# Kernel tuning notes

Measured on AMD Instinct MI355X. Metric: run time of the kernel, lower is better.

Reference implementation:

```python
import jax, jax.numpy as jnp
import numpy as np

M0, M1, H = 128, 64, 8            # scalar mul, vector mul, num heads
AH0, AH1 = 16, 8                  # per-head irreps: 16x0e + 8x1e
D = M0 + 3 * M1                   # 320 node feature dim
DTP0 = M0 + M1                    # 192 scalar channels out of depthwise TP
DTP1 = M0 + 2 * M1                # 256 vector channels out of depthwise TP
WNUM = 2 * M0 + 3 * M1            # 448 TP path weights (uvu, edge mul=1)
RAD_IN, RAD_HID = 32, 64
N_NODES, N_EDGES = 10000, 160000
INV_SQRT3 = 1.0 / np.sqrt(3.0)    # CG norm for 1e x 1e -> 0e
INV_SQRT2 = 1.0 / np.sqrt(2.0)    # CG norm for 1e x 1e -> 1e


def _split(x, m0, m1):
    # e3nn layout: [m0 scalars | m1 vectors * 3 components]
    return x[..., :m0], x[..., m0:].reshape(x.shape[:-1] + (m1, 3))


def _silu(x):
    return x * jax.nn.sigmoid(x)


def _smooth_leaky(x, a=0.2):
    # SmoothLeakyReLU from equiformer
    return 0.5 * (1 + a) * x + 0.5 * (1 - a) * x * (2.0 * jax.nn.sigmoid(x) - 1.0)


def _dtp(s, v, e0, e1, w):
    # depthwise (uvu) tensor product of (M0x0e + M1x1e) with edge attr (1x0e + 1x1e)
    # s [E,M0], v [E,M1,3], e0 [E,1], e1 [E,3], w [E,WNUM] or [WNUM] (internal)
    w1, w2, w3, w4, w5 = jnp.split(w, [M0, 2 * M0, 2 * M0 + M1, 2 * M0 + 2 * M1], axis=-1)
    os1 = w1 * s * e0                                                  # 0e x 0e -> 0e
    os2 = w4 * (jnp.einsum('emc,ec->em', v, e1) * INV_SQRT3)           # 1e x 1e -> 0e
    ov1 = (w2 * s)[..., None] * e1[:, None, :]                         # 0e x 1e -> 1e
    ov2 = w3[..., None] * v * e0[..., None]                            # 1e x 0e -> 1e
    ov3 = w5[..., None] * (jnp.cross(v, e1[:, None, :]) * INV_SQRT2)   # 1e x 1e -> 1e
    return jnp.concatenate([os1, os2], -1), jnp.concatenate([ov1, ov2, ov3], -2)


def _forward(node_input, edge_src, edge_dst, edge_attr, edge_scalars,
             Wsrc_s, Wsrc_v, bsrc, Wdst_s, Wdst_v,
             rad_W1, rad_b1, rad_W2, rad_off,
             Wact_s, bact, Wact_v, Walpha, balpha, w_int,
             Wval_s, bval, Wval_v, alpha_dot, Wproj_s, bproj, Wproj_v):
    N = node_input.shape[0]
    E = edge_src.shape[0]
    s, v = _split(node_input, M0, M1)
    # merge_src / merge_dst: per-irrep linear (bias only on scalars of src)
    ms_s = s @ Wsrc_s + bsrc
    ms_v = jnp.einsum('nmc,mk->nkc', v, Wsrc_v)
    md_s = s @ Wdst_s
    md_v = jnp.einsum('nmc,mk->nkc', v, Wdst_v)
    msg_s = ms_s[edge_src] + md_s[edge_dst]          # [E, M0]
    msg_v = ms_v[edge_src] + md_v[edge_dst]          # [E, M1, 3]
    e0, e1 = edge_attr[:, :1], edge_attr[:, 1:4]
    # radial profile MLP -> edge-dependent TP weights
    w = _silu(edge_scalars @ rad_W1 + rad_b1) @ rad_W2 + rad_off       # [E, WNUM]
    ds, dv = _dtp(msg_s, msg_v, e0, e1, w)           # [E, DTP0], [E, DTP1, 3]
    # alpha branch: linear on TP scalars -> heads -> smooth leaky -> dot
    al = _smooth_leaky((ds @ Walpha + balpha).reshape(E, H, AH0))
    logits = jnp.einsum('ehk,hk->eh', al, alpha_dot[0])                # [E, H]
    # value branch: sep_act.lin + gate
    scal = ds @ Wact_s + bact                        # [E, M0+M1] scalars+gates
    gated_v = jnp.einsum('emc,mk->ekc', dv, Wact_v)  # [E, M1, 3]
    val_s = _silu(scal[:, :M0])
    val_v = gated_v * jax.nn.sigmoid(scal[:, M0:])[..., None]
    # sep_value: depthwise TP with internal weights + linear
    vs, vv = _dtp(val_s, val_v, e0, e1, w_int)
    out_s = vs @ Wval_s + bval                       # [E, H*AH0]
    out_v = jnp.einsum('emc,mk->ekc', vv, Wval_v)    # [E, H*AH1, 3]
    value = jnp.concatenate([out_s.reshape(E, H, AH0),
                             out_v.reshape(E, H, AH1 * 3)], axis=2)    # [E, H, 40]
    # softmax over incoming edges per destination node
    mx = jax.lax.stop_gradient(jax.ops.segment_max(logits, edge_dst, num_segments=N))
    mx = jnp.where(jnp.isfinite(mx), mx, 0.0)
    ex = jnp.exp(logits - mx[edge_dst])
    den = jax.ops.segment_sum(ex, edge_dst, num_segments=N)
    alpha = ex / (den[edge_dst] + 1e-16)             # [E, H]
    agg = jax.ops.segment_sum(value * alpha[..., None], edge_dst, num_segments=N)
    # heads2vec + output projection
    node_s = agg[:, :, :AH0].reshape(N, H * AH0)
    node_v = agg[:, :, AH0:].reshape(N, H * AH1, 3)
    po_s = node_s @ Wproj_s + bproj
    po_v = jnp.einsum('nmc,mk->nkc', node_v, Wproj_v)
    return jnp.concatenate([po_s, po_v.reshape(N, M1 * 3)], axis=1)


def _lin(key, fi, fo):
    return jax.random.normal(key, (fi, fo), jnp.float32) / np.sqrt(fi)


def setup_inputs() -> dict:
    ks = iter(jax.random.split(jax.random.key(0), 40))
    inp = {}
    inp['node_input'] = jax.random.normal(next(ks), (N_NODES, D), jnp.float32)
    inp['edge_src'] = jax.random.randint(next(ks), (N_EDGES,), 0, N_NODES)
    inp['edge_dst'] = jax.random.randint(next(ks), (N_EDGES,), 0, N_NODES)
    inp['edge_attr'] = jax.random.normal(next(ks), (N_EDGES, 4), jnp.float32)
    inp['edge_scalars'] = jax.random.normal(next(ks), (N_EDGES, RAD_IN), jnp.float32)
    inp['Wsrc_s'] = _lin(next(ks), M0, M0)
    inp['Wsrc_v'] = _lin(next(ks), M1, M1)
    inp['bsrc'] = 0.1 * jax.random.normal(next(ks), (M0,), jnp.float32)
    inp['Wdst_s'] = _lin(next(ks), M0, M0)
    inp['Wdst_v'] = _lin(next(ks), M1, M1)
    inp['rad_W1'] = _lin(next(ks), RAD_IN, RAD_HID)
    inp['rad_b1'] = 0.1 * jax.random.normal(next(ks), (RAD_HID,), jnp.float32)
    inp['rad_W2'] = _lin(next(ks), RAD_HID, WNUM)
    inp['rad_off'] = 0.1 * jax.random.normal(next(ks), (WNUM,), jnp.float32)
    inp['Wact_s'] = _lin(next(ks), DTP0, M0 + M1)
    inp['bact'] = 0.1 * jax.random.normal(next(ks), (M0 + M1,), jnp.float32)
    inp['Wact_v'] = _lin(next(ks), DTP1, M1)
    inp['Walpha'] = _lin(next(ks), DTP0, H * AH0)
    inp['balpha'] = 0.1 * jax.random.normal(next(ks), (H * AH0,), jnp.float32)
    inp['w_int'] = jax.random.normal(next(ks), (WNUM,), jnp.float32)
    inp['Wval_s'] = _lin(next(ks), DTP0, H * AH0)
    inp['bval'] = 0.1 * jax.random.normal(next(ks), (H * AH0,), jnp.float32)
    inp['Wval_v'] = _lin(next(ks), DTP1, H * AH1)
    inp['alpha_dot'] = jax.random.normal(next(ks), (1, H, AH0), jnp.float32) / np.sqrt(AH0)
    inp['Wproj_s'] = _lin(next(ks), H * AH0, M0)
    inp['bproj'] = 0.1 * jax.random.normal(next(ks), (M0,), jnp.float32)
    inp['Wproj_v'] = _lin(next(ks), H * AH1, M1)
    return inp


def reference(node_input, edge_src, edge_dst, edge_attr, edge_scalars,
              Wsrc_s, Wsrc_v, bsrc, Wdst_s, Wdst_v,
              rad_W1, rad_b1, rad_W2, rad_off,
              Wact_s, bact, Wact_v, Walpha, balpha, w_int,
              Wval_s, bval, Wval_v, alpha_dot, Wproj_s, bproj, Wproj_v):
    return _forward(node_input, edge_src, edge_dst, edge_attr, edge_scalars,
                    Wsrc_s, Wsrc_v, bsrc, Wdst_s, Wdst_v,
                    rad_W1, rad_b1, rad_W2, rad_off,
                    Wact_s, bact, Wact_v, Walpha, balpha, w_int,
                    Wval_s, bval, Wval_v, alpha_dot, Wproj_s, bproj, Wproj_v)
```

## Files before the change

kernel.cpp:

```cpp
#include <hip/hip_runtime.h>

#define NN 10000
#define NE 160000
#define INV_SQRT3f 0.57735026918962576f
#define INV_SQRT2f 0.70710678118654752f

typedef short bshort8 __attribute__((ext_vector_type(8)));
typedef float floatx4 __attribute__((ext_vector_type(4)));
#define MFMA16(a,b,c) __builtin_amdgcn_mfma_f32_16x16x32_bf16((a),(b),(c),0,0,0)

__device__ __forceinline__ float sigm(float x){ return 1.f/(1.f+__expf(-x)); }
__device__ __forceinline__ float siluf(float x){ return x*sigm(x); }
__device__ __forceinline__ float sleaky(float x){ return 0.6f*x + 0.4f*x*(2.f*sigm(x)-1.f); }
__device__ __forceinline__ unsigned short f2bf(float f){
  return (unsigned short)((__float_as_uint(f) + 0x8000u)>>16);
}
__device__ __forceinline__ float bf2f(unsigned short h){
  return __uint_as_float(((unsigned)h)<<16);
}
__device__ __forceinline__ unsigned cvtpk(float lo, float hi){
  unsigned r;
  asm("v_cvt_pk_bf16_f32 %0, %1, %2" : "=v"(r) : "v"(lo), "v"(hi));
  return r;
}
__device__ __forceinline__ float lo16f(unsigned u){ return __uint_as_float(u<<16); }
__device__ __forceinline__ float hi16f(unsigned u){ return __uint_as_float(u & 0xffff0000u); }

#define O_W1   0
#define O_W2   2048
#define O_WAS  30720
#define O_WAVT 67584
#define O_WAVB 75776
#define O_WVS  83968
#define O_WVVT 108544
#define O_WVVB 116736
#define O_WALP 124928
#define SWZ_TOTAL 149504

__global__ __launch_bounds__(256) void k_pre_all(
    const float* __restrict__ x,
    const float* __restrict__ Wsrc_s, const float* __restrict__ Wsrc_v,
    const float* __restrict__ bsrc,
    const float* __restrict__ Wdst_s, const float* __restrict__ Wdst_v,
    unsigned short* __restrict__ ms_s, unsigned short* __restrict__ md_s,
    unsigned short* __restrict__ ms_v, unsigned short* __restrict__ md_v,
    const float* __restrict__ W1, const float* __restrict__ W2,
    const float* __restrict__ WAs, const float* __restrict__ WAv,
    const float* __restrict__ WVs, const float* __restrict__ WVv,
    const float* __restrict__ WAl, const float* __restrict__ w_int,
    unsigned short* __restrict__ swz,
    float* __restrict__ num, float* __restrict__ den, int* __restrict__ cnt) {
  __shared__ __align__(16) float s_s[128*16];
  __shared__ __align__(16) float s_v[192*16];
  const int tid = threadIdx.x;
  const int b = blockIdx.x;
  if (b >= 1209) {
    int base = (b-1209)*256 + tid;
    float4 z = {0.f,0.f,0.f,0.f};
    for (int i = base; i < 800000; i += 554496) ((float4*)num)[i] = z;
    if (base < 20000) ((float4*)den)[base] = z;
    if (base < 10000) cnt[base] = 0;
    return;
  }
  if (b >= 625) {
    int s = (b-625)*256 + tid;
    if (s >= SWZ_TOTAL) return;
    const float* src; int base, N, KT, rowOff;
    if      (s < 2048)  { base=O_W1;   src=W1;  N=64;  KT=1; rowOff=0; }
    else if (s < 30720) { base=O_W2;   src=W2;  N=448; KT=2; rowOff=0; }
    else if (s < 67584) { base=O_WAS;  src=WAs; N=192; KT=6; rowOff=0; }
    else if (s < 75776) { base=O_WAVT; src=WAv; N=64;  KT=4; rowOff=0; }
    else if (s < 83968) { base=O_WAVB; src=WAv; N=64;  KT=4; rowOff=128; }
    else if (s < 108544){ base=O_WVS;  src=WVs; N=128; KT=6; rowOff=0; }
    else if (s < 116736){ base=O_WVVT; src=WVv; N=64;  KT=4; rowOff=0; }
    else if (s < 124928){ base=O_WVVB; src=WVv; N=64;  KT=4; rowOff=128; }
    else                { base=O_WALP; src=WAl; N=128; KT=6; rowOff=0; }
    int loc = s - base;
    int j = loc & 7, l = (loc>>3)&63, kt = (loc>>9)%KT, nt = loc/(512*KT);
    int row = kt*32 + (l>>4)*8 + j + rowOff;
    int col = nt*16 + (l&15);
    float scl = 1.f;
    if      (base == O_WVS)  scl = (row < 128) ? w_int[row] : w_int[192+row]*INV_SQRT3f;
    else if (base == O_WVVT) scl = w_int[128+row];
    else if (base == O_WVVB) scl = (row < 192) ? w_int[128+row] : w_int[192+row]*INV_SQRT2f;
    swz[s] = f2bf(src[row*N + col] * scl);
    return;
  }
  const int n0 = b*16;
  for (int idx = tid; idx < 16*320; idx += 256) {
    int n = idx/320, d = idx - n*320;
    float val = x[(n0+n)*320 + d];
    if (d < 128) s_s[d*16+n] = val;
    else         s_v[(d-128)*16+n] = val;
  }
  __syncthreads();
  {
    int g = tid>>7, j = tid&127;
    float accs[8], accd[8];
    float bb = bsrc[j];
    #pragma unroll
    for (int i=0;i<8;i++){ accs[i]=bb; accd[i]=0.f; }
    for (int k=0;k<128;k++) {
      float w1 = Wsrc_s[k*128+j], w2 = Wdst_s[k*128+j];
      float4 a0 = *(const float4*)&s_s[k*16+g*8];
      float4 a1 = *(const float4*)&s_s[k*16+g*8+4];
      accs[0]+=a0.x*w1; accs[1]+=a0.y*w1; accs[2]+=a0.z*w1; accs[3]+=a0.w*w1;
      accs[4]+=a1.x*w1; accs[5]+=a1.y*w1; accs[6]+=a1.z*w1; accs[7]+=a1.w*w1;
      accd[0]+=a0.x*w2; accd[1]+=a0.y*w2; accd[2]+=a0.z*w2; accd[3]+=a0.w*w2;
      accd[4]+=a1.x*w2; accd[5]+=a1.y*w2; accd[6]+=a1.z*w2; accd[7]+=a1.w*w2;
    }
    #pragma unroll
    for (int i=0;i<8;i++){ int n=n0+g*8+i; ms_s[n*128+j]=f2bf(accs[i]); md_s[n*128+j]=f2bf(accd[i]); }
  }
  if (tid < 192) {
    int c = tid>>6, k = tid&63;
    #pragma unroll
    for (int half=0; half<2; ++half) {
      float accs[8], accd[8];
      #pragma unroll
      for (int e=0;e<8;e++){ accs[e]=0.f; accd[e]=0.f; }
      for (int m=0;m<64;m++) {
        float w1 = Wsrc_v[m*64+k], w2 = Wdst_v[m*64+k];
        float4 v0 = *(const float4*)&s_v[(m*3+c)*16 + half*8];
        float4 v1 = *(const float4*)&s_v[(m*3+c)*16 + half*8 + 4];
        accs[0]+=v0.x*w1; accs[1]+=v0.y*w1; accs[2]+=v0.z*w1; accs[3]+=v0.w*w1;
        accs[4]+=v1.x*w1; accs[5]+=v1.y*w1; accs[6]+=v1.z*w1; accs[7]+=v1.w*w1;
        accd[0]+=v0.x*w2; accd[1]+=v0.y*w2; accd[2]+=v0.z*w2; accd[3]+=v0.w*w2;
        accd[4]+=v1.x*w2; accd[5]+=v1.y*w2; accd[6]+=v1.z*w2; accd[7]+=v1.w*w2;
      }
      #pragma unroll
      for (int e=0;e<8;e++){
        int n = n0 + half*8 + e;
        ms_v[(n*64+k)*4 + c] = f2bf(accs[e]);
        md_v[(n*64+k)*4 + c] = f2bf(accd[e]);
      }
    }
  }
}

__global__ __launch_bounds__(256) void k_hist(const int* __restrict__ edst,
                                              int* __restrict__ cnt) {
  int e = blockIdx.x*256 + threadIdx.x;
  if (e < NE) atomicAdd(&cnt[edst[e]], 1);
}

__global__ __launch_bounds__(256) void k_scan(const int* __restrict__ cnt,
                                              int* __restrict__ offs) {
  __shared__ int sc[10240];
  __shared__ int wsum[4];
  const int tid = threadIdx.x;
  const int lane = tid & 63, wave = tid >> 6;
  for (int i = tid; i < 10240; i += 256) sc[i] = (i < NN) ? cnt[i] : 0;
  __syncthreads();
  int v[40]; int s = 0;
  #pragma unroll
  for (int j=0;j<40;j++){ v[j] = sc[tid*40+j]; s += v[j]; }
  int incl = s;
  #pragma unroll
  for (int d=1; d<64; d<<=1) { int t = __shfl_up(incl, d, 64); if (lane>=d) incl += t; }
  if (lane==63) wsum[wave] = incl;
  __syncthreads();
  int wbase = 0;
  for (int w=0; w<wave; ++w) wbase += wsum[w];
  int excl = wbase + incl - s;
  #pragma unroll
  for (int j=0;j<40;j++){ int i = tid*40+j; if (i<NN) offs[i] = excl; excl += v[j]; }
}

__global__ __launch_bounds__(256) void k_scatter(const int* __restrict__ edst,
                                                 int* __restrict__ offs,
                                                 int* __restrict__ perm) {
  int e = blockIdx.x*256 + threadIdx.x;
  if (e < NE) {
    int pos = atomicAdd(&offs[edst[e]], 1);
    perm[pos] = e;
  }
}

__global__ __launch_bounds__(256, 6) void e_all(
    const unsigned short* __restrict__ ms_s, const unsigned short* __restrict__ md_s,
    const unsigned short* __restrict__ ms_v, const unsigned short* __restrict__ md_v,
    const int* __restrict__ esrc, const int* __restrict__ edst,
    const int* __restrict__ perm,
    const float* __restrict__ eattr, const float* __restrict__ escal,
    const float* __restrict__ rad_b1, const float* __restrict__ rad_off,
    const float* __restrict__ bact,
    const float* __restrict__ bval,
    const float* __restrict__ balpha, const float* __restrict__ alpha_dot,
    const unsigned short* __restrict__ swz,
    float* __restrict__ den, float* __restrict__ num) {
  __shared__ __align__(16) char smem[24768];
  unsigned short* ads  = (unsigned short*)smem;
  unsigned short* at1  = (unsigned short*)(smem+6400);
  unsigned short* advb = (unsigned short*)(smem+10752);
  unsigned short* aes  = (unsigned short*)(smem+10752);
  unsigned short* ah   = (unsigned short*)(smem+12032);
  float* vout          = (float*)(smem+10752);
  float* s_e0 = (float*)(smem+23808);
  float* s_e1 = (float*)(smem+23872);
  float* s_ex = (float*)(smem+24064);
  int* s_eid  = (int*)(smem+24576);
  int* s_src  = (int*)(smem+24640);
  int* s_dst  = (int*)(smem+24704);
  const int tid  = threadIdx.x;
  const int lane = tid & 63, wave = tid >> 6;
  const int quad = lane >> 4, l15 = lane & 15;
  const int bswz = (blockIdx.x & 7)*1250 + (blockIdx.x >> 3);
  const int eb = bswz*16;

  if (tid < 16) {
    int eid = perm[eb+tid];
    s_eid[tid] = eid; s_src[tid] = esrc[eid]; s_dst[tid] = edst[eid];
  }
  __syncthreads();
  if (tid >= 64 && tid < 128) {
    int t = tid-64, e = t>>2, q = t&3;
    float a = eattr[s_eid[e]*4+q];
    if (q == 0) s_e0[e] = a; else s_e1[(q-1)*16+e] = a;
  }
  {
    int e = tid>>4, i0 = (tid&15)*2;
    float2 es = *(const float2*)&escal[s_eid[e]*32+i0];
    *(unsigned*)&aes[e*40+i0] = cvtpk(es.x, es.y);
  }
  __syncthreads();

  {
    int nt = wave, col = nt*16 + l15;
    bshort8 a = *(const bshort8*)&aes[l15*40 + quad*8];
    bshort8 b = *(const bshort8*)&swz[O_W1 + (nt*64 + lane)*8];
    float bb = rad_b1[col];
    floatx4 acc = {bb,bb,bb,bb};
    acc = MFMA16(a, b, acc);
    #pragma unroll
    for (int r=0;r<4;r++) ah[(quad*4+r)*72 + col] = f2bf(siluf(acc[r]));
  }
  __syncthreads();

  {
    bshort8 ha0 = *(const bshort8*)&ah[l15*72 + quad*8];
    bshort8 ha1 = *(const bshort8*)&ah[l15*72 + 32 + quad*8];
    __syncthreads();
    int src_[4], dst_[4];
    #pragma unroll
    for (int r=0;r<4;r++){ int e=quad*4+r; src_[r]=s_src[e]; dst_[r]=s_dst[e]; }
    #pragma unroll
    for (int p=0;p<2;p++) {
      int nt1 = wave*2+p, nt2 = nt1+8;
      int m = nt1*16 + l15;
      float o1 = rad_off[m], o2 = rad_off[128+m];
      floatx4 a1 = {o1,o1,o1,o1}, a2 = {o2,o2,o2,o2};
      a1 = MFMA16(ha0, *(const bshort8*)&swz[O_W2 + ((nt1*2+0)*64+lane)*8], a1);
      a1 = MFMA16(ha1, *(const bshort8*)&swz[O_W2 + ((nt1*2+1)*64+lane)*8], a1);
      a2 = MFMA16(ha0, *(const bshort8*)&swz[O_W2 + ((nt2*2+0)*64+lane)*8], a2);
      a2 = MFMA16(ha1, *(const bshort8*)&swz[O_W2 + ((nt2*2+1)*64+lane)*8], a2);
      #pragma unroll
      for (int r=0;r<4;r++) {
        int e = quad*4+r;
        float msgs = bf2f(ms_s[src_[r]*128+m]) + bf2f(md_s[dst_[r]*128+m]);
        ads[e*200+m] = f2bf(a1[r]*msgs*s_e0[e]);
        at1[e*136+m] = f2bf(a2[r]*msgs);
      }
    }
    floatx4 aw3, aw4, aw5;
    {
      int nt = 16 + wave; float o = rad_off[nt*16+l15];
      floatx4 acc = {o,o,o,o};
      acc = MFMA16(ha0, *(const bshort8*)&swz[O_W2 + ((nt*2+0)*64+lane)*8], acc);
      acc = MFMA16(ha1, *(const bshort8*)&swz[O_W2 + ((nt*2+1)*64+lane)*8], acc);
      aw3 = acc;
    }
    {
      int nt = 20 + wave; float o = rad_off[nt*16+l15];
      floatx4 acc = {o,o,o,o};
      acc = MFMA16(ha0, *(const bshort8*)&swz[O_W2 + ((nt*2+0)*64+lane)*8], acc);
      acc = MFMA16(ha1, *(const bshort8*)&swz[O_W2 + ((nt*2+1)*64+lane)*8], acc);
      aw4 = acc;
    }
    {
      int nt = 24 + wave; float o = rad_off[nt*16+l15];
      floatx4 acc = {o,o,o,o};
      acc = MFMA16(ha0, *(const bshort8*)&swz[O_W2 + ((nt*2+0)*64+lane)*8], acc);
      acc = MFMA16(ha1, *(const bshort8*)&swz[O_W2 + ((nt*2+1)*64+lane)*8], acc);
      aw5 = acc;
    }
    const int k = wave*16 + l15;
    #pragma unroll
    for (int r=0;r<4;r++) {
      int e = quad*4 + r;
      uint2 us = *(const uint2*)&ms_v[(src_[r]*64 + k)*4];
      uint2 ud = *(const uint2*)&md_v[(dst_[r]*64 + k)*4];
      float vx = lo16f(us.x) + lo16f(ud.x);
      float vy = hi16f(us.x) + hi16f(ud.x);
      float vz = lo16f(us.y) + lo16f(ud.y);
      float ex1 = s_e1[0+e], ey1 = s_e1[16+e], ez1 = s_e1[32+e];
      float e0 = s_e0[e];
      float d = vx*ex1 + vy*ey1 + vz*ez1;
      ads[e*200+128+k] = f2bf(aw4[r]*d*INV_SQRT3f);
      float w3v = aw3[r]*e0;
      float w5  = aw5[r]*INV_SQRT2f;
      advb[0*2176 + e*136 + k] = f2bf(w3v*vx);
      advb[1*2176 + e*136 + k] = f2bf(w3v*vy);
      advb[2*2176 + e*136 + k] = f2bf(w3v*vz);
      advb[0*2176 + e*136 + 64+k] = f2bf(w5*(vy*ez1 - vz*ey1));
      advb[1*2176 + e*136 + 64+k] = f2bf(w5*(vz*ex1 - vx*ez1));
      advb[2*2176 + e*136 + 64+k] = f2bf(w5*(vx*ey1 - vy*ex1));
    }
  }
  __syncthreads();

  floatx4 sc0, sc1, sc2, gsa, gb0, gb1, gb2;
  {
    bshort8 fa[6];
    #pragma unroll
    for (int kt=0;kt<6;kt++) fa[kt] = *(const bshort8*)&ads[l15*200 + kt*32 + quad*8];
    #pragma unroll
    for (int t=0;t<2;t++) {
      int h = wave*2 + t;
      int col = h*16 + l15;
      float bb = balpha[col];
      floatx4 acc = {bb,bb,bb,bb};
      #pragma unroll
      for (int kt=0;kt<6;kt++)
        acc = MFMA16(fa[kt], *(const bshort8*)&swz[O_WALP + ((h*6+kt)*64+lane)*8], acc);
      float ad = alpha_dot[col];
      float exv[4];
      #pragma unroll
      for (int r=0;r<4;r++) {
        float p = sleaky(acc[r])*ad;
        p += __shfl_xor(p, 1);
        p += __shfl_xor(p, 2);
        p += __shfl_xor(p, 4);
        p += __shfl_xor(p, 8);
        float ex = __expf(p);
        exv[r] = ex;
        if (l15 == 0) s_ex[(quad*4+r)*8+h] = ex;
      }
      if (l15 == 0) {
        float racc = exv[0]; int cur = s_dst[quad*4];
        #pragma unroll
        for (int r=1;r<4;r++) {
          int d = s_dst[quad*4+r];
          if (d != cur) { atomicAdd(&den[cur*8+h], racc); racc = 0.f; cur = d; }
          racc += exv[r];
        }
        atomicAdd(&den[cur*8+h], racc);
      }
    }
    {
      float bb = bact[wave*16 + l15];
      floatx4 a0 = {bb,bb,bb,bb};
      #pragma unroll
      for (int kt=0;kt<6;kt++)
        a0 = MFMA16(fa[kt], *(const bshort8*)&swz[O_WAS + ((wave*6+kt)*64+lane)*8], a0);
      sc0 = a0;
    }
    {
      float bb = bact[(wave+4)*16 + l15];
      floatx4 a1 = {bb,bb,bb,bb};
      #pragma unroll
      for (int kt=0;kt<6;kt++)
        a1 = MFMA16(fa[kt], *(const bshort8*)&swz[O_WAS + (((wave+4)*6+kt)*64+lane)*8], a1);
      sc1 = a1;
    }
    {
      float bb = bact[(wave+8)*16 + l15];
      floatx4 a2 = {bb,bb,bb,bb};
      #pragma unroll
      for (int kt=0;kt<6;kt++)
        a2 = MFMA16(fa[kt], *(const bshort8*)&swz[O_WAS + (((wave+8)*6+kt)*64+lane)*8], a2);
      sc2 = a2;
    }
    bshort8 ft[4];
    #pragma unroll
    for (int kt=0;kt<4;kt++) ft[kt] = *(const bshort8*)&at1[l15*136 + kt*32 + quad*8];
    {
      floatx4 acc = {0.f,0.f,0.f,0.f};
      #pragma unroll
      for (int kt=0;kt<4;kt++)
        acc = MFMA16(ft[kt], *(const bshort8*)&swz[O_WAVT + ((wave*4+kt)*64+lane)*8], acc);
      gsa = acc;
    }
    {
      bshort8 wb[4];
      #pragma unroll
      for (int kt=0;kt<4;kt++) wb[kt] = *(const bshort8*)&swz[O_WAVB + ((wave*4+kt)*64+lane)*8];
      #pragma unroll
      for (int c=0;c<3;c++) {
        floatx4 acc = {0.f,0.f,0.f,0.f};
        #pragma unroll
        for (int kt=0;kt<4;kt++) {
          bshort8 fb = *(const bshort8*)&advb[c*2176 + l15*136 + kt*32 + quad*8];
          acc = MFMA16(fb, wb[kt], acc);
        }
        if (c==0) gb0 = acc; else if (c==1) gb1 = acc; else gb2 = acc;
      }
    }
  }
  __syncthreads();

  {
    const int k = wave*16 + l15;
    #pragma unroll
    for (int r=0;r<4;r++) {
      int row = quad*4 + r;
      float e0 = s_e0[row];
      {
        float v = siluf(sc0[r]);
        ads[row*200+k] = f2bf(v*e0);
        at1[row*136+k] = f2bf(v);
      }
      {
        float v = siluf(sc1[r]);
        ads[row*200+64+k] = f2bf(v*e0);
        at1[row*136+64+k] = f2bf(v);
      }
      {
        float sg = sigm(sc2[r]);
        float gs = gsa[r];
        float ex1 = s_e1[0+row], ey1 = s_e1[16+row], ez1 = s_e1[32+row];
        float v0 = (gs*ex1 + gb0[r])*sg;
        float v1 = (gs*ey1 + gb1[r])*sg;
        float v2 = (gs*ez1 + gb2[r])*sg;
        float d = v0*ex1 + v1*ey1 + v2*ez1;
        ads[row*200+128+k] = f2bf(d);
        advb[0*2176 + row*136 + k] = f2bf(v0*e0);
        advb[1*2176 + row*136 + k] = f2bf(v1*e0);
        advb[2*2176 + row*136 + k] = f2bf(v2*e0);
        advb[0*2176 + row*136 + 64+k] = f2bf(v1*ez1 - v2*ey1);
        advb[1*2176 + row*136 + 64+k] = f2bf(v2*ex1 - v0*ez1);
        advb[2*2176 + row*136 + 64+k] = f2bf(v0*ey1 - v1*ex1);
      }
    }
  }
  __syncthreads();

  {
    bshort8 ft[4];
    #pragma unroll
    for (int kt=0;kt<4;kt++) ft[kt] = *(const bshort8*)&at1[l15*136 + kt*32 + quad*8];
    floatx4 vsh = {0.f,0.f,0.f,0.f};
    #pragma unroll
    for (int kt=0;kt<4;kt++)
      vsh = MFMA16(ft[kt], *(const bshort8*)&swz[O_WVVT + ((wave*4+kt)*64+lane)*8], vsh);
    floatx4 vb0, vb1, vb2;
    {
      bshort8 wb[4];
      #pragma unroll
      for (int kt=0;kt<4;kt++) wb[kt] = *(const bshort8*)&swz[O_WVVB + ((wave*4+kt)*64+lane)*8];
      #pragma unroll
      for (int c=0;c<3;c++) {
        floatx4 acc = {0.f,0.f,0.f,0.f};
        #pragma unroll
        for (int kt=0;kt<4;kt++) {
          bshort8 fb = *(const bshort8*)&advb[c*2176 + l15*136 + kt*32 + quad*8];
          acc = MFMA16(fb, wb[kt], acc);
        }
        if (c==0) vb0 = acc; else if (c==1) vb1 = acc; else vb2 = acc;
      }
    }
    __syncthreads();
    const int k = wave*16 + l15;
    const int h = k>>3, q = k&7;
    #pragma unroll
    for (int r=0;r<4;r++) {
      int row = quad*4 + r;
      float exr = s_ex[row*8+h];
      vout[row*194 + h*24 + q*3 + 0] = (vb0[r] + s_e1[0*16+row]*vsh[r])*exr;
      vout[row*194 + h*24 + q*3 + 1] = (vb1[r] + s_e1[1*16+row]*vsh[r])*exr;
      vout[row*194 + h*24 + q*3 + 2] = (vb2[r] + s_e1[2*16+row]*vsh[r])*exr;
    }
  }
  __syncthreads();

  if (tid < 192) {
    const int jj = tid;
    const int h = jj/24, rr = jj - h*24;
    float acc = 0.f; int cur = s_dst[0];
    #pragma unroll
    for (int e = 0; e < 16; ++e) {
      int d = s_dst[e];
      if (d != cur) { atomicAdd(&num[cur*320 + h*40 + 16 + rr], acc); acc = 0.f; cur = d; }
      acc += vout[e*194 + jj];
    }
    atomicAdd(&num[cur*320 + h*40 + 16 + rr], acc);
  }
  __syncthreads();

  {
    bshort8 fa[6];
    #pragma unroll
    for (int kt=0;kt<6;kt++) fa[kt] = *(const bshort8*)&ads[l15*200 + kt*32 + quad*8];
    #pragma unroll
    for (int t=0;t<2;t++) {
      int h = wave + 4*t;
      float bb = bval[h*16 + l15];
      floatx4 acc = {bb,bb,bb,bb};
      #pragma unroll
      for (int kt=0;kt<6;kt++)
        acc = MFMA16(fa[kt], *(const bshort8*)&swz[O_WVS + ((h*6+kt)*64+lane)*8], acc);
      #pragma unroll
      for (int r=0;r<4;r++) {
        int row = quad*4 + r;
        vout[row*132 + h*16 + l15] = acc[r]*s_ex[row*8+h];
      }
    }
  }
  __syncthreads();

  if (tid < 128) {
    const int j = tid, h = j>>4, jj = j&15;
    float acc = 0.f; int cur = s_dst[0];
    #pragma unroll
    for (int e = 0; e < 16; ++e) {
      int d = s_dst[e];
      if (d != cur) { atomicAdd(&num[cur*320 + h*40 + jj], acc); acc = 0.f; cur = d; }
      acc += vout[e*132 + j];
    }
    atomicAdd(&num[cur*320 + h*40 + jj], acc);
  }
}

__global__ __launch_bounds__(256) void node_post(
    const float* __restrict__ num, const float* __restrict__ den,
    const float* __restrict__ Wproj_s, const float* __restrict__ bproj,
    const float* __restrict__ Wproj_v, float* __restrict__ out) {
  __shared__ __align__(16) float s_ns[128*16];
  __shared__ __align__(16) float s_nv[192*16];
  const int tid = threadIdx.x;
  const int n0 = blockIdx.x*16;
  for (int idx = tid; idx < 16*320; idx += 256) {
    int n = idx/320, j = idx - n*320;
    int h = j/40, r = j - h*40;
    float a = num[(n0+n)*320+j] / (den[(n0+n)*8+h] + 1e-16f);
    if (r < 16) s_ns[(h*16+r)*16+n] = a;
    else        s_nv[(h*24 + (r-16))*16+n] = a;
  }
  __syncthreads();
  {
    int g = tid>>7, j = tid&127;
    float acc[8]; float b = bproj[j];
    #pragma unroll
    for (int i=0;i<8;i++) acc[i]=b;
    for (int k=0;k<128;k++) {
      float wv = Wproj_s[k*128+j];
      float4 a0 = *(const float4*)&s_ns[k*16+g*8];
      float4 a1 = *(const float4*)&s_ns[k*16+g*8+4];
      acc[0]+=a0.x*wv; acc[1]+=a0.y*wv; acc[2]+=a0.z*wv; acc[3]+=a0.w*wv;
      acc[4]+=a1.x*wv; acc[5]+=a1.y*wv; acc[6]+=a1.z*wv; acc[7]+=a1.w*wv;
    }
    #pragma unroll
    for (int i=0;i<8;i++) out[(n0+g*8+i)*320 + j] = acc[i];
  }
  if (tid < 192) {
    int c = tid>>6, k = tid&63;
    #pragma unroll
    for (int half=0; half<2; ++half) {
      float acc[8];
      #pragma unroll
      for (int e=0;e<8;e++) acc[e]=0.f;
      for (int m=0;m<64;m++) {
        float wv = Wproj_v[m*64+k];
        float4 v0 = *(const float4*)&s_nv[(m*3+c)*16 + half*8];
        float4 v1 = *(const float4*)&s_nv[(m*3+c)*16 + half*8 + 4];
        acc[0]+=v0.x*wv; acc[1]+=v0.y*wv; acc[2]+=v0.z*wv; acc[3]+=v0.w*wv;
        acc[4]+=v1.x*wv; acc[5]+=v1.y*wv; acc[6]+=v1.z*wv; acc[7]+=v1.w*wv;
      }
      #pragma unroll
      for (int e=0;e<8;e++) out[(n0+half*8+e)*320 + 128 + k*3 + c] = acc[e];
    }
  }
}

extern "C" void kernel_launch(void* const* d_in, const int* in_sizes, int n_in,
                              void* d_out, int out_size, void* d_ws, size_t ws_size,
                              hipStream_t stream) {
  (void)in_sizes; (void)n_in; (void)out_size; (void)ws_size;
  const float* node_input = (const float*)d_in[0];
  const int*   esrc       = (const int*)d_in[1];
  const int*   edst       = (const int*)d_in[2];
  const float* eattr      = (const float*)d_in[3];
  const float* escal      = (const float*)d_in[4];
  const float* Wsrc_s     = (const float*)d_in[5];
  const float* Wsrc_v     = (const float*)d_in[6];
  const float* bsrc       = (const float*)d_in[7];
  const float* Wdst_s     = (const float*)d_in[8];
  const float* Wdst_v     = (const float*)d_in[9];
  const float* rad_W1     = (const float*)d_in[10];
  const float* rad_b1     = (const float*)d_in[11];
  const float* rad_W2     = (const float*)d_in[12];
  const float* rad_off    = (const float*)d_in[13];
  const float* Wact_s     = (const float*)d_in[14];
  const float* bact       = (const float*)d_in[15];
  const float* Wact_v     = (const float*)d_in[16];
  const float* Walpha     = (const float*)d_in[17];
  const float* balpha     = (const float*)d_in[18];
  const float* w_int      = (const float*)d_in[19];
  const float* Wval_s     = (const float*)d_in[20];
  const float* bval       = (const float*)d_in[21];
  const float* Wval_v     = (const float*)d_in[22];
  const float* alpha_dot  = (const float*)d_in[23];
  const float* Wproj_s    = (const float*)d_in[24];
  const float* bproj      = (const float*)d_in[25];
  const float* Wproj_v    = (const float*)d_in[26];
  float* out = (float*)d_out;

  char* wsb = (char*)d_ws;
  unsigned short* ms_s16 = (unsigned short*)(wsb);
  unsigned short* md_s16 = (unsigned short*)(wsb + 2560000);
  unsigned short* ms_v4  = (unsigned short*)(wsb + 5120000);
  unsigned short* md_v4  = (unsigned short*)(wsb + 10240000);
  float* den             = (float*)(wsb + 15360000);
  float* num             = (float*)(wsb + 15680000);
  unsigned short* swz    = (unsigned short*)(wsb + 28480000);
  int* cnt  = (int*)(wsb + 28779008);
  int* offs = (int*)(wsb + 28819008);
  int* perm = (int*)(wsb + 28859008);

  k_pre_all<<<3375, 256, 0, stream>>>(node_input, Wsrc_s, Wsrc_v, bsrc, Wdst_s, Wdst_v,
                                      ms_s16, md_s16, ms_v4, md_v4,
                                      rad_W1, rad_W2, Wact_s, Wact_v, Wval_s, Wval_v,
                                      Walpha, w_int, swz, num, den, cnt);
  k_hist<<<625, 256, 0, stream>>>(edst, cnt);
  k_scan<<<1, 256, 0, stream>>>(cnt, offs);
  k_scatter<<<625, 256, 0, stream>>>(edst, offs, perm);
  e_all<<<10000, 256, 0, stream>>>(ms_s16, md_s16, ms_v4, md_v4, esrc, edst, perm, eattr, escal,
                                   rad_b1, rad_off, bact, bval,
                                   balpha, alpha_dot, swz, den, num);
  node_post<<<625, 256, 0, stream>>>(num, den, Wproj_s, bproj, Wproj_v, out);
}
```

Before: 441.0 us.

## Store merged vector features planar and stage vector weights through shared memory

Merged src/dst vector features change from padded xyz4 interleaved storage to three planar bf16 arrays. This removes the padding slot and cuts gather bytes by a quarter. The w3/w4/w5 radial weights are now staged to LDS, and the vector tensor-product step is rewritten so each thread handles two channels with packed bf16 converts. The scalar value path and its atomics move earlier, and some barriers are reordered. LDS use grows and the occupancy hint drops from 6 to 5 blocks per SM, which may reduce latency hiding.

```diff
diff --git a/kernel.cpp b/kernel.cpp
--- a/kernel.cpp
+++ b/kernel.cpp
@@ -4,6 +4,7 @@
 #define NE 160000
 #define INV_SQRT3f 0.57735026918962576f
 #define INV_SQRT2f 0.70710678118654752f
+#define VPLU 640000
 
 typedef short bshort8 __attribute__((ext_vector_type(8)));
 typedef float floatx4 __attribute__((ext_vector_type(4)));
@@ -131,8 +132,8 @@
       #pragma unroll
       for (int e=0;e<8;e++){
         int n = n0 + half*8 + e;
-        ms_v[(n*64+k)*4 + c] = f2bf(accs[e]);
-        md_v[(n*64+k)*4 + c] = f2bf(accd[e]);
+        ms_v[c*VPLU + n*64 + k] = f2bf(accs[e]);
+        md_v[c*VPLU + n*64 + k] = f2bf(accd[e]);
       }
     }
   }
@@ -177,7 +178,7 @@
   }
 }
 
-__global__ __launch_bounds__(256, 6) void e_all(
+__global__ __launch_bounds__(256, 5) void e_all(
     const unsigned short* __restrict__ ms_s, const unsigned short* __restrict__ md_s,
     const unsigned short* __restrict__ ms_v, const unsigned short* __restrict__ md_v,
     const int* __restrict__ esrc, const int* __restrict__ edst,
@@ -189,19 +190,20 @@
     const float* __restrict__ balpha, const float* __restrict__ alpha_dot,
     const unsigned short* __restrict__ swz,
     float* __restrict__ den, float* __restrict__ num) {
-  __shared__ __align__(16) char smem[24768];
-  unsigned short* ads  = (unsigned short*)smem;
-  unsigned short* at1  = (unsigned short*)(smem+6400);
-  unsigned short* advb = (unsigned short*)(smem+10752);
-  unsigned short* aes  = (unsigned short*)(smem+10752);
-  unsigned short* ah   = (unsigned short*)(smem+12032);
-  float* vout          = (float*)(smem+10752);
-  float* s_e0 = (float*)(smem+23808);
-  float* s_e1 = (float*)(smem+23872);
-  float* s_ex = (float*)(smem+24064);
-  int* s_eid  = (int*)(smem+24576);
-  int* s_src  = (int*)(smem+24640);
-  int* s_dst  = (int*)(smem+24704);
+  __shared__ __align__(16) char smem[30912];
+  unsigned short* sw_v = (unsigned short*)smem;
+  float* vout          = (float*)smem;
+  unsigned short* ads  = (unsigned short*)(smem+6144);
+  unsigned short* at1  = (unsigned short*)(smem+12544);
+  unsigned short* advb = (unsigned short*)(smem+16896);
+  unsigned short* aes  = (unsigned short*)(smem+16896);
+  unsigned short* ah   = (unsigned short*)(smem+19456);
+  float* s_e0 = (float*)(smem+29952);
+  float* s_e1 = (float*)(smem+30016);
+  float* s_ex = (float*)(smem+30208);
+  int* s_eid  = (int*)(smem+30720);
+  int* s_src  = (int*)(smem+30784);
+  int* s_dst  = (int*)(smem+30848);
   const int tid  = threadIdx.x;
   const int lane = tid & 63, wave = tid >> 6;
   const int quad = lane >> 4, l15 = lane & 15;
@@ -240,7 +242,6 @@
   {
     bshort8 ha0 = *(const bshort8*)&ah[l15*72 + quad*8];
     bshort8 ha1 = *(const bshort8*)&ah[l15*72 + 32 + quad*8];
-    __syncthreads();
     int src_[4], dst_[4];
     #pragma unroll
     for (int r=0;r<4;r++){ int e=quad*4+r; src_[r]=s_src[e]; dst_[r]=s_dst[e]; }
@@ -262,50 +263,54 @@
         at1[e*136+m] = f2bf(a2[r]*msgs);
       }
     }
-    floatx4 aw3, aw4, aw5;
-    {
-      int nt = 16 + wave; float o = rad_off[nt*16+l15];
+    #pragma unroll
+    for (int q=0;q<3;q++) {
+      int nt = 16 + wave*3 + q, col = nt*16 + l15;
+      float o = rad_off[col];
       floatx4 acc = {o,o,o,o};
       acc = MFMA16(ha0, *(const bshort8*)&swz[O_W2 + ((nt*2+0)*64+lane)*8], acc);
       acc = MFMA16(ha1, *(const bshort8*)&swz[O_W2 + ((nt*2+1)*64+lane)*8], acc);
-      aw3 = acc;
-    }
-    {
-      int nt = 20 + wave; float o = rad_off[nt*16+l15];
-      floatx4 acc = {o,o,o,o};
-      acc = MFMA16(ha0, *(const bshort8*)&swz[O_W2 + ((nt*2+0)*64+lane)*8], acc);
-      acc = MFMA16(ha1, *(const bshort8*)&swz[O_W2 + ((nt*2+1)*64+lane)*8], acc);
-      aw4 = acc;
-    }
-    {
-      int nt = 24 + wave; float o = rad_off[nt*16+l15];
-      floatx4 acc = {o,o,o,o};
-      acc = MFMA16(ha0, *(const bshort8*)&swz[O_W2 + ((nt*2+0)*64+lane)*8], acc);
-      acc = MFMA16(ha1, *(const bshort8*)&swz[O_W2 + ((nt*2+1)*64+lane)*8], acc);
-      aw5 = acc;
-    }
-    const int k = wave*16 + l15;
-    #pragma unroll
-    for (int r=0;r<4;r++) {
-      int e = quad*4 + r;
-      uint2 us = *(const uint2*)&ms_v[(src_[r]*64 + k)*4];
-      uint2 ud = *(const uint2*)&md_v[(dst_[r]*64 + k)*4];
-      float vx = lo16f(us.x) + lo16f(ud.x);
-      float vy = hi16f(us.x) + hi16f(ud.x);
-      float vz = lo16f(us.y) + lo16f(ud.y);
-      float ex1 = s_e1[0+e], ey1 = s_e1[16+e], ez1 = s_e1[32+e];
-      float e0 = s_e0[e];
-      float d = vx*ex1 + vy*ey1 + vz*ez1;
-      ads[e*200+128+k] = f2bf(aw4[r]*d*INV_SQRT3f);
-      float w3v = aw3[r]*e0;
-      float w5  = aw5[r]*INV_SQRT2f;
-      advb[0*2176 + e*136 + k] = f2bf(w3v*vx);
-      advb[1*2176 + e*136 + k] = f2bf(w3v*vy);
-      advb[2*2176 + e*136 + k] = f2bf(w3v*vz);
-      advb[0*2176 + e*136 + 64+k] = f2bf(w5*(vy*ez1 - vz*ey1));
-      advb[1*2176 + e*136 + 64+k] = f2bf(w5*(vz*ex1 - vx*ez1));
-      advb[2*2176 + e*136 + 64+k] = f2bf(w5*(vx*ey1 - vy*ex1));
-    }
+      #pragma unroll
+      for (int r=0;r<4;r++) sw_v[(quad*4+r)*192 + (col-256)] = f2bf(acc[r]);
+    }
+  }
+  __syncthreads();
+
+  #pragma unroll
+  for (int it = 0; it < 2; ++it) {
+    int t = tid + it*256;
+    int e = t>>5, pr = t&31;
+    int k0 = pr*2;
+    int sb = s_src[e]*64 + k0, db = s_dst[e]*64 + k0;
+    unsigned usx = *(const unsigned*)&ms_v[0*VPLU+sb];
+    unsigned usy = *(const unsigned*)&ms_v[1*VPLU+sb];
+    unsigned usz = *(const unsigned*)&ms_v[2*VPLU+sb];
+    unsigned udx = *(const unsigned*)&md_v[0*VPLU+db];
+    unsigned udy = *(const unsigned*)&md_v[1*VPLU+db];
+    unsigned udz = *(const unsigned*)&md_v[2*VPLU+db];
+    unsigned uw3 = *(const unsigned*)&sw_v[e*192 + k0];
+    unsigned uw4 = *(const unsigned*)&sw_v[e*192 + 64 + k0];
+    unsigned uw5 = *(const unsigned*)&sw_v[e*192 + 128 + k0];
+    float ex1 = s_e1[0+e], ey1 = s_e1[16+e], ez1 = s_e1[32+e];
+    float e0 = s_e0[e];
+    float vx0 = lo16f(usx)+lo16f(udx), vx1 = hi16f(usx)+hi16f(udx);
+    float vy0 = lo16f(usy)+lo16f(udy), vy1 = hi16f(usy)+hi16f(udy);
+    float vz0 = lo16f(usz)+lo16f(udz), vz1 = hi16f(usz)+hi16f(udz);
+    float d0 = vx0*ex1 + vy0*ey1 + vz0*ez1;
+    float d1 = vx1*ex1 + vy1*ey1 + vz1*ez1;
+    *(unsigned*)&ads[e*200+128+k0] =
+        cvtpk(lo16f(uw4)*d0*INV_SQRT3f, hi16f(uw4)*d1*INV_SQRT3f);
+    float w30 = lo16f(uw3)*e0, w31 = hi16f(uw3)*e0;
+    float w50 = lo16f(uw5)*INV_SQRT2f, w51 = hi16f(uw5)*INV_SQRT2f;
+    *(unsigned*)&advb[0*2176 + e*136 + k0] = cvtpk(w30*vx0, w31*vx1);
+    *(unsigned*)&advb[1*2176 + e*136 + k0] = cvtpk(w30*vy0, w31*vy1);
+    *(unsigned*)&advb[2*2176 + e*136 + k0] = cvtpk(w30*vz0, w31*vz1);
+    *(unsigned*)&advb[0*2176 + e*136 + 64+k0] =
+        cvtpk(w50*(vy0*ez1 - vz0*ey1), w51*(vy1*ez1 - vz1*ey1));
+    *(unsigned*)&advb[1*2176 + e*136 + 64+k0] =
+        cvtpk(w50*(vz0*ex1 - vx0*ez1), w51*(vz1*ex1 - vx1*ez1));
+    *(unsigned*)&advb[2*2176 + e*136 + 64+k0] =
+        cvtpk(w50*(vx0*ey1 - vy0*ex1), w51*(vx1*ey1 - vy1*ex1));
   }
   __syncthreads();
 
@@ -436,6 +441,41 @@
   __syncthreads();
 
   {
+    bshort8 fa[6];
+    #pragma unroll
+    for (int kt=0;kt<6;kt++) fa[kt] = *(const bshort8*)&ads[l15*200 + kt*32 + quad*8];
+    __syncthreads();
+    #pragma unroll
+    for (int t=0;t<2;t++) {
+      int h = wave + 4*t;
+      float bb = bval[h*16 + l15];
+      floatx4 acc = {bb,bb,bb,bb};
+      #pragma unroll
+      for (int kt=0;kt<6;kt++)
+        acc = MFMA16(fa[kt], *(const bshort8*)&swz[O_WVS + ((h*6+kt)*64+lane)*8], acc);
+      #pragma unroll
+      for (int r=0;r<4;r++) {
+        int row = quad*4 + r;
+        vout[row*132 + h*16 + l15] = acc[r]*s_ex[row*8+h];
+      }
+    }
+  }
+  __syncthreads();
+
+  if (tid < 128) {
+    const int j = tid, h = j>>4, jj = j&15;
+    float acc = 0.f; int cur = s_dst[0];
+    #pragma unroll
+    for (int e = 0; e < 16; ++e) {
+      int d = s_dst[e];
+      if (d != cur) { atomicAdd(&num[cur*320 + h*40 + jj], acc); acc = 0.f; cur = d; }
+      acc += vout[e*132 + j];
+    }
+    atomicAdd(&num[cur*320 + h*40 + jj], acc);
+  }
+  __syncthreads();
+
+  {
     bshort8 ft[4];
     #pragma unroll
     for (int kt=0;kt<4;kt++) ft[kt] = *(const bshort8*)&at1[l15*136 + kt*32 + quad*8];
@@ -443,6 +483,8 @@
     #pragma unroll
     for (int kt=0;kt<4;kt++)
       vsh = MFMA16(ft[kt], *(const bshort8*)&swz[O_WVVT + ((wave*4+kt)*64+lane)*8], vsh);
+    const int k = wave*16 + l15;
+    const int h = k>>3, q = k&7;
     floatx4 vb0, vb1, vb2;
     {
       bshort8 wb[4];
@@ -459,9 +501,6 @@
         if (c==0) vb0 = acc; else if (c==1) vb1 = acc; else vb2 = acc;
       }
     }
-    __syncthreads();
-    const int k = wave*16 + l15;
-    const int h = k>>3, q = k&7;
     #pragma unroll
     for (int r=0;r<4;r++) {
       int row = quad*4 + r;
@@ -484,40 +523,6 @@
       acc += vout[e*194 + jj];
     }
     atomicAdd(&num[cur*320 + h*40 + 16 + rr], acc);
-  }
-  __syncthreads();
-
-  {
-    bshort8 fa[6];
-    #pragma unroll
-    for (int kt=0;kt<6;kt++) fa[kt] = *(const bshort8*)&ads[l15*200 + kt*32 + quad*8];
-    #pragma unroll
-    for (int t=0;t<2;t++) {
-      int h = wave + 4*t;
-      float bb = bval[h*16 + l15];
-      floatx4 acc = {bb,bb,bb,bb};
-      #pragma unroll
-      for (int kt=0;kt<6;kt++)
-        acc = MFMA16(fa[kt], *(const bshort8*)&swz[O_WVS + ((h*6+kt)*64+lane)*8], acc);
-      #pragma unroll
-      for (int r=0;r<4;r++) {
-        int row = quad*4 + r;
-        vout[row*132 + h*16 + l15] = acc[r]*s_ex[row*8+h];
-      }
-    }
-  }
-  __syncthreads();
-
-  if (tid < 128) {
-    const int j = tid, h = j>>4, jj = j&15;
-    float acc = 0.f; int cur = s_dst[0];
-    #pragma unroll
-    for (int e = 0; e < 16; ++e) {
-      int d = s_dst[e];
-      if (d != cur) { atomicAdd(&num[cur*320 + h*40 + jj], acc); acc = 0.f; cur = d; }
-      acc += vout[e*132 + j];
-    }
-    atomicAdd(&num[cur*320 + h*40 + jj], acc);
   }
 }
 
@@ -608,23 +613,23 @@
   char* wsb = (char*)d_ws;
   unsigned short* ms_s16 = (unsigned short*)(wsb);
   unsigned short* md_s16 = (unsigned short*)(wsb + 2560000);
-  unsigned short* ms_v4  = (unsigned short*)(wsb + 5120000);
-  unsigned short* md_v4  = (unsigned short*)(wsb + 10240000);
-  float* den             = (float*)(wsb + 15360000);
-  float* num             = (float*)(wsb + 15680000);
-  unsigned short* swz    = (unsigned short*)(wsb + 28480000);
-  int* cnt  = (int*)(wsb + 28779008);
-  int* offs = (int*)(wsb + 28819008);
-  int* perm = (int*)(wsb + 28859008);
+  unsigned short* ms_v16 = (unsigned short*)(wsb + 5120000);
+  unsigned short* md_v16 = (unsigned short*)(wsb + 8960000);
+  float* den             = (float*)(wsb + 12800000);
+  float* num             = (float*)(wsb + 13120000);
+  unsigned short* swz    = (unsigned short*)(wsb + 25920000);
+  int* cnt  = (int*)(wsb + 26220032);
+  int* offs = (int*)(wsb + 26260032);
+  int* perm = (int*)(wsb + 26300032);
 
   k_pre_all<<<3375, 256, 0, stream>>>(node_input, Wsrc_s, Wsrc_v, bsrc, Wdst_s, Wdst_v,
-                                      ms_s16, md_s16, ms_v4, md_v4,
+                                      ms_s16, md_s16, ms_v16, md_v16,
                                       rad_W1, rad_W2, Wact_s, Wact_v, Wval_s, Wval_v,
                                       Walpha, w_int, swz, num, den, cnt);
   k_hist<<<625, 256, 0, stream>>>(edst, cnt);
   k_scan<<<1, 256, 0, stream>>>(cnt, offs);
   k_scatter<<<625, 256, 0, stream>>>(edst, offs, perm);
-  e_all<<<10000, 256, 0, stream>>>(ms_s16, md_s16, ms_v4, md_v4, esrc, edst, perm, eattr, escal,
+  e_all<<<10000, 256, 0, stream>>>(ms_s16, md_s16, ms_v16, md_v16, esrc, edst, perm, eattr, escal,
                                    rad_b1, rad_off, bact, bval,
                                    balpha, alpha_dot, swz, den, num);
   node_post<<<625, 256, 0, stream>>>(num, den, Wproj_s, bproj, Wproj_v, out);
```

New measurement: 382.3 us. 13.3% less time.
